# Kernel optimization log

Hardware: AMD Instinct MI355X
Metric: run time of the kernel (lower is better)

Reference implementation:

```python
import jax, jax.numpy as jnp
import numpy as np

E, D, DIM, H, DH, MLP = 8, 6, 512, 8, 64, 512
P, S, NC, B = 4, 32, 10, 128
PD = 3 * P * P          # patch_dim = 48
GRID = S // P           # 8
N = GRID * GRID + 1     # 65 tokens (64 patches + cls)


def setup_inputs() -> dict:
    key = jax.random.key(0)
    ks = iter(jax.random.split(key, 16))
    r = lambda *s: jax.random.normal(next(ks), s, jnp.float32) * 0.02
    z = lambda *s: jnp.zeros(s, jnp.float32)
    o = lambda *s: jnp.ones(s, jnp.float32)
    return dict(
        x=jax.random.normal(next(ks), (B, 3, S, S), jnp.float32),
        gate_w=r(E, 3 * S * S), gate_b=z(E),
        pln1_g=o(E, PD), pln1_b=z(E, PD),
        patch_w=r(E, PD, DIM), patch_b=z(E, DIM),
        pln2_g=o(E, DIM), pln2_b=z(E, DIM),
        cls_tok=r(E, DIM), pos_emb=r(E, N, DIM),
        aln_g=o(E, D, DIM), aln_b=z(E, D, DIM),
        qkv_w=r(E, D, DIM, 3 * H * DH),
        out_w=r(E, D, H * DH, DIM), out_b=z(E, D, DIM),
        fln_g=o(E, D, DIM), fln_b=z(E, D, DIM),
        ff1_w=r(E, D, DIM, MLP), ff1_b=z(E, D, MLP),
        ff2_w=r(E, D, MLP, DIM), ff2_b=z(E, D, DIM),
        final_g=o(E, DIM), final_b=z(E, DIM),
        head_w=r(E, DIM, NC), head_b=z(E, NC))


def _ln(x, g, b):
    m = x.mean(-1, keepdims=True)
    v = ((x - m) ** 2).mean(-1, keepdims=True)
    return (x - m) * jax.lax.rsqrt(v + 1e-5) * g + b


LAYER_KEYS = ('aln_g', 'aln_b', 'qkv_w', 'out_w', 'out_b',
              'fln_g', 'fln_b', 'ff1_w', 'ff1_b', 'ff2_w', 'ff2_b')


def _vit(x, p):
    # x: [B, 3, S, S]; p: per-expert param dict (no leading expert axis)
    Bx = x.shape[0]
    # rearrange 'b c (h p1) (w p2) -> b (h w) (p1 p2 c)'
    t = x.reshape(Bx, 3, GRID, P, GRID, P).transpose(0, 2, 4, 3, 5, 1)
    t = t.reshape(Bx, GRID * GRID, PD)
    t = _ln(t, p['pln1_g'], p['pln1_b'])
    t = t @ p['patch_w'] + p['patch_b']
    t = _ln(t, p['pln2_g'], p['pln2_b'])
    cls = jnp.broadcast_to(p['cls_tok'][None, None, :], (Bx, 1, DIM))
    t = jnp.concatenate([cls, t], axis=1) + p['pos_emb'][None]  # [B, N, DIM]

    def block(t, lp):
        g = _ln(t, lp['aln_g'], lp['aln_b'])
        qkv = g @ lp['qkv_w']                       # [B, N, 3*H*DH]
        q, k, v = jnp.split(qkv, 3, axis=-1)
        q = q.reshape(Bx, N, H, DH).transpose(0, 2, 1, 3)
        k = k.reshape(Bx, N, H, DH).transpose(0, 2, 1, 3)
        v = v.reshape(Bx, N, H, DH).transpose(0, 2, 1, 3)
        att = jax.nn.softmax(jnp.einsum('bhid,bhjd->bhij', q, k) * (DH ** -0.5), axis=-1)
        o = jnp.einsum('bhij,bhjd->bhid', att, v).transpose(0, 2, 1, 3).reshape(Bx, N, H * DH)
        t = t + o @ lp['out_w'] + lp['out_b']
        g = _ln(t, lp['fln_g'], lp['fln_b'])
        f = jax.nn.gelu(g @ lp['ff1_w'] + lp['ff1_b'], approximate=False) @ lp['ff2_w'] + lp['ff2_b']
        return t + f, None

    layer_p = {k: p[k] for k in LAYER_KEYS}  # each [D, ...]
    t, _ = jax.lax.scan(block, t, layer_p)
    t = _ln(t, p['final_g'], p['final_b'])
    return t[:, 0] @ p['head_w'] + p['head_b']   # [B, NC]


def _moe(x, params):
    Bx = x.shape[0]
    logits = x.reshape(Bx, -1) @ params['gate_w'].T + params['gate_b']  # [B, E]
    top1 = jnp.argmax(logits, axis=1)                                   # [B]
    expert_p = {k: v for k, v in params.items() if k not in ('gate_w', 'gate_b')}
    all_out = jax.vmap(lambda pp: _vit(x, pp))(expert_p)                # [E, B, NC]
    return all_out[top1, jnp.arange(Bx)]                                # [B, NC]


def reference(x, gate_w, gate_b, pln1_g, pln1_b, patch_w, patch_b, pln2_g, pln2_b,
              cls_tok, pos_emb, aln_g, aln_b, qkv_w, out_w, out_b,
              fln_g, fln_b, ff1_w, ff1_b, ff2_w, ff2_b, final_g, final_b,
              head_w, head_b):
    params = {k: v for k, v in locals().items() if k != 'x'}
    return _moe(x, params)
```

## Files before the change

### kernel.cpp

```cpp
#include <hip/hip_runtime.h>
#include <math.h>

#define EXPERTS 8
#define DEPTH 6
#define DIM 512
#define HEADS 8
#define NCLS 10
#define BATCH 128
#define PD 48
#define NTOK 65
#define NRT256 40
#define NRT128 80
#define NROWSP (NRT256 * 256)

typedef __attribute__((ext_vector_type(4))) float f32x4;
typedef __attribute__((ext_vector_type(8))) __bf16 bf16x8;
typedef unsigned short u16;

#define GLOAD_LDS16(gp, lp)                                                     \
    __builtin_amdgcn_global_load_lds(                                           \
        (const __attribute__((address_space(1))) void*)(gp),                    \
        (__attribute__((address_space(3))) void*)(lp), 16, 0, 0)

__device__ inline u16 f2bf(float f) {
    union { float f; unsigned u; } v; v.f = f;
    unsigned r = v.u + 0x7FFFu + ((v.u >> 16) & 1u);
    return (u16)(r >> 16);
}
__device__ inline float bf2f(u16 s) {
    union { unsigned u; float f; } v; v.u = ((unsigned)s) << 16;
    return v.f;
}

__global__ __launch_bounds__(256) void gate_k(const float* __restrict__ x,
                                              const float* __restrict__ gw,
                                              const float* __restrict__ gb,
                                              int* __restrict__ top1) {
    int b = blockIdx.x, tid = threadIdx.x;
    const float* xb = x + (size_t)b * 3072;
    float acc[EXPERTS];
#pragma unroll
    for (int e = 0; e < EXPERTS; ++e) acc[e] = 0.f;
    for (int i = tid; i < 3072; i += 256) {
        float xv = xb[i];
#pragma unroll
        for (int e = 0; e < EXPERTS; ++e)
            acc[e] = fmaf(xv, gw[(size_t)e * 3072 + i], acc[e]);
    }
    __shared__ float red[256];
    __shared__ float logits[EXPERTS];
    for (int e = 0; e < EXPERTS; ++e) {
        red[tid] = acc[e];
        __syncthreads();
        for (int s = 128; s > 0; s >>= 1) {
            if (tid < s) red[tid] += red[tid + s];
            __syncthreads();
        }
        if (tid == 0) logits[e] = red[0] + gb[e];
        __syncthreads();
    }
    if (tid == 0) {
        int best = 0;
        float bv = logits[0];
        for (int e = 1; e < EXPERTS; ++e)
            if (logits[e] > bv) { bv = logits[e]; best = e; }
        top1[b] = best;
    }
}

__global__ __launch_bounds__(128) void route3_k(const int* __restrict__ top1,
                                                int* __restrict__ prow,
                                                int* __restrict__ tile_e) {
    __shared__ int t1[BATCH];
    int tid = threadIdx.x;
    t1[tid] = top1[tid];
    __syncthreads();
    if (tid != 0) return;
    int row = 0, tile = 0;
    for (int e = 0; e < EXPERTS; ++e) {
        int ne = 0;
        for (int b = 0; b < BATCH; ++b)
            if (t1[b] == e) { prow[b] = row + ne * 65; ne++; }
        if (!ne) continue;
        int nt = (ne * 65 + 255) >> 8;
        for (int tt = 0; tt < nt; ++tt) tile_e[tile++] = e;
        row += nt << 8;
    }
    for (; tile < NRT256; ++tile) tile_e[tile] = -1;
}

__global__ __launch_bounds__(256) void patch_k(const float* __restrict__ x,
                                               const float* __restrict__ pln1_g,
                                               const float* __restrict__ pln1_b,
                                               const float* __restrict__ patch_w,
                                               const float* __restrict__ patch_b,
                                               const float* __restrict__ pln2_g,
                                               const float* __restrict__ pln2_b,
                                               const float* __restrict__ cls_tok,
                                               const float* __restrict__ pos_emb,
                                               const int* __restrict__ top1,
                                               const int* __restrict__ prow,
                                               float* __restrict__ t) {
    int n = blockIdx.x, b = blockIdx.y, tid = threadIdx.x;
    int e = top1[b];
    float* trow = t + ((size_t)prow[b] + n) * DIM;
    const float* pe = pos_emb + ((size_t)e * NTOK + n) * DIM;

    if (n == 0) {
        for (int d = tid; d < DIM; d += 256)
            trow[d] = cls_tok[e * DIM + d] + pe[d];
        return;
    }
    int pi = n - 1, h = pi >> 3, w = pi & 7;
    __shared__ float pv[PD];
    __shared__ float red[256];
    if (tid < PD) {
        int p1 = tid / 12, rem = tid % 12, p2 = rem / 3, c = rem % 3;
        pv[tid] = x[((size_t)b * 3 + c) * 1024 + (h * 4 + p1) * 32 + (w * 4 + p2)];
    }
    __syncthreads();
    float m = 0.f, q = 0.f;
    for (int j = 0; j < PD; ++j) { float v = pv[j]; m += v; q += v * v; }
    m *= (1.f / PD);
    q = q * (1.f / PD) - m * m;
    float rs = rsqrtf(q + 1e-5f);
    __syncthreads();
    if (tid < PD)
        pv[tid] = (pv[tid] - m) * rs * pln1_g[e * PD + tid] + pln1_b[e * PD + tid];
    __syncthreads();

    float acc0 = patch_b[e * DIM + tid];
    float acc1 = patch_b[e * DIM + tid + 256];
    for (int j = 0; j < PD; ++j) {
        float v = pv[j];
        const float* wr = patch_w + ((size_t)e * PD + j) * DIM;
        acc0 = fmaf(v, wr[tid], acc0);
        acc1 = fmaf(v, wr[tid + 256], acc1);
    }
    red[tid] = acc0 + acc1;
    __syncthreads();
    for (int s = 128; s > 0; s >>= 1) {
        if (tid < s) red[tid] += red[tid + s];
        __syncthreads();
    }
    float S = red[0];
    __syncthreads();
    red[tid] = acc0 * acc0 + acc1 * acc1;
    __syncthreads();
    for (int s = 128; s > 0; s >>= 1) {
        if (tid < s) red[tid] += red[tid + s];
        __syncthreads();
    }
    float Q = red[0];
    float mean = S * (1.f / DIM);
    float var = Q * (1.f / DIM) - mean * mean;
    float rs2 = rsqrtf(var + 1e-5f);
    trow[tid]       = (acc0 - mean) * rs2 * pln2_g[e * DIM + tid]       + pln2_b[e * DIM + tid]       + pe[tid];
    trow[tid + 256] = (acc1 - mean) * rs2 * pln2_g[e * DIM + tid + 256] + pln2_b[e * DIM + tid + 256] + pe[tid + 256];
}

__global__ __launch_bounds__(256) void ln2_k(const float* __restrict__ src,
                                             u16* __restrict__ dst,
                                             const float* __restrict__ gbase,
                                             const float* __restrict__ bbase,
                                             const int* __restrict__ tile_e,
                                             int gestride) {
    int row = blockIdx.x * 4 + (threadIdx.x >> 6);
    int lane = threadIdx.x & 63;
    int e = tile_e[row >> 8];
    if (e < 0) return;
    const float* s = src + (size_t)row * 512;
    float4 a = *(const float4*)&s[lane * 4];
    float4 b = *(const float4*)&s[256 + lane * 4];
    float sum = a.x + a.y + a.z + a.w + b.x + b.y + b.z + b.w;
    float sq = a.x * a.x + a.y * a.y + a.z * a.z + a.w * a.w +
               b.x * b.x + b.y * b.y + b.z * b.z + b.w * b.w;
#pragma unroll
    for (int off = 32; off > 0; off >>= 1) {
        sum += __shfl_xor(sum, off);
        sq += __shfl_xor(sq, off);
    }
    float mean = sum * (1.f / DIM);
    float rs = rsqrtf(sq * (1.f / DIM) - mean * mean + 1e-5f);
    const float* g = gbase + (size_t)e * gestride;
    const float* bb = bbase + (size_t)e * gestride;
    float4 g0 = *(const float4*)&g[lane * 4];
    float4 g1 = *(const float4*)&g[256 + lane * 4];
    float4 b0 = *(const float4*)&bb[lane * 4];
    float4 b1 = *(const float4*)&bb[256 + lane * 4];
    int swz = (row & 7) << 3;
    u16 o[4];
    o[0] = f2bf((a.x - mean) * rs * g0.x + b0.x);
    o[1] = f2bf((a.y - mean) * rs * g0.y + b0.y);
    o[2] = f2bf((a.z - mean) * rs * g0.z + b0.z);
    o[3] = f2bf((a.w - mean) * rs * g0.w + b0.w);
    *(int2*)&dst[(size_t)row * 512 + ((lane * 4) ^ swz)] = *(int2*)o;
    o[0] = f2bf((b.x - mean) * rs * g1.x + b1.x);
    o[1] = f2bf((b.y - mean) * rs * g1.y + b1.y);
    o[2] = f2bf((b.z - mean) * rs * g1.z + b1.z);
    o[3] = f2bf((b.w - mean) * rs * g1.w + b1.w);
    *(int2*)&dst[(size_t)row * 512 + ((256 + lane * 4) ^ swz)] = *(int2*)o;
}

__global__ __launch_bounds__(256) void wconv_k(const float* __restrict__ src,
                                               u16* __restrict__ dst, int N) {
    __shared__ float tile[32][33];
    int n0 = blockIdx.x * 32, k0 = blockIdx.y * 32, m = blockIdx.z;
    const float* s = src + (size_t)m * 512 * N;
    u16* d = dst + (size_t)m * 512 * N;
    int r = threadIdx.x >> 5, c = threadIdx.x & 31;
#pragma unroll
    for (int i = 0; i < 4; ++i)
        tile[r + i * 8][c] = s[(size_t)(k0 + r + i * 8) * N + n0 + c];
    __syncthreads();
#pragma unroll
    for (int i = 0; i < 4; ++i) {
        int n = n0 + r + i * 8;
        d[(size_t)n * 512 + ((k0 + c) ^ ((n & 7) << 3))] = f2bf(tile[c][r + i * 8]);
    }
}

__global__ __launch_bounds__(512) void mgemm6_k(const u16* __restrict__ A,
                                                const u16* __restrict__ Wtbase,
                                                u16* __restrict__ C,
                                                const int* __restrict__ tile_e,
                                                int westride) {
    constexpr int N = 1536, CT = 12;
    int orig = blockIdx.x, nwg = NRT256 * CT;
    int q = nwg >> 3, r8 = nwg & 7;
    int xcd = orig & 7, off = orig >> 3;
    int wg = (xcd < r8 ? xcd * (q + 1) : r8 * (q + 1) + (xcd - r8) * q) + off;
    int tile = wg / CT, ct = wg - tile * CT;
    int e = tile_e[tile];
    if (e < 0) return;
    int row0 = tile * 256, c0 = ct * 128;
    const u16* Wt = Wtbase + (size_t)e * westride;

    int tid = threadIdx.x;
    int lane = tid & 63, w = tid >> 6;
    int rl = lane & 15, kg = lane >> 4;
    int wr = w >> 1, wc = w & 1;

    __shared__ __align__(16) u16 As[256 * 64];
    __shared__ __align__(16) u16 Bs[128 * 64];

    f32x4 acc[4][4];
#pragma unroll
    for (int mt = 0; mt < 4; ++mt)
#pragma unroll
        for (int nt = 0; nt < 4; ++nt) acc[mt][nt] = (f32x4){0.f, 0.f, 0.f, 0.f};

    const u16* Ag = A + (size_t)(row0 + w * 32 + (lane >> 3)) * 512 + (lane & 7) * 8;
    const u16* Bg = Wt + (size_t)(c0 + w * 16 + (lane >> 3)) * 512 + (lane & 7) * 8;
    u16* Asw = As + w * 2048;
    u16* Bsw = Bs + w * 1024;

    int blk0 = (kg ^ (rl & 7)) * 8;
    int blk1 = ((4 + kg) ^ (rl & 7)) * 8;

    for (int k0 = 0; k0 < 512; k0 += 64) {
#pragma unroll
        for (int i = 0; i < 4; ++i)
            GLOAD_LDS16(Ag + k0 + i * 8 * 512, Asw + i * 512);
#pragma unroll
        for (int i = 0; i < 2; ++i)
            GLOAD_LDS16(Bg + k0 + i * 8 * 512, Bsw + i * 512);
        __syncthreads();
#pragma unroll
        for (int ks = 0; ks < 2; ++ks) {
            int blk = ks ? blk1 : blk0;
            bf16x8 av[4], bv[4];
#pragma unroll
            for (int i = 0; i < 4; ++i) {
                av[i] = *(const bf16x8*)&As[(wr * 64 + i * 16 + rl) * 64 + blk];
                bv[i] = *(const bf16x8*)&Bs[(wc * 64 + i * 16 + rl) * 64 + blk];
            }
#pragma unroll
            for (int mt = 0; mt < 4; ++mt)
#pragma unroll
                for (int nt = 0; nt < 4; ++nt)
                    acc[mt][nt] = __builtin_amdgcn_mfma_f32_16x16x32_bf16(
                        av[mt], bv[nt], acc[mt][nt], 0, 0, 0);
        }
        __syncthreads();
    }

    int rh = lane >> 4;
#pragma unroll
    for (int mt = 0; mt < 4; ++mt)
#pragma unroll
        for (int nt = 0; nt < 4; ++nt)
#pragma unroll
            for (int rr = 0; rr < 4; ++rr) {
                size_t grow = row0 + wr * 64 + mt * 16 + rh * 4 + rr;
                int c = c0 + wc * 64 + nt * 16 + rl;
                C[grow * N + c] = f2bf(acc[mt][nt][rr]);
            }
}

template <int OP>
__global__ __launch_bounds__(256) void mgemm5_k(const u16* __restrict__ A,
                                                const u16* __restrict__ Wtbase,
                                                const float* __restrict__ Bbase,
                                                void* __restrict__ Cptr,
                                                const int* __restrict__ tile_e,
                                                int westride, int bestride) {
    constexpr int CT = 4;
    int orig = blockIdx.x, nwg = NRT128 * CT;
    int q = nwg >> 3, r8 = nwg & 7;
    int xcd = orig & 7, off = orig >> 3;
    int wg = (xcd < r8 ? xcd * (q + 1) : r8 * (q + 1) + (xcd - r8) * q) + off;
    int tile = wg / CT, ct = wg - tile * CT;
    int e = tile_e[tile >> 1];
    if (e < 0) return;
    int row0 = tile * 128, c0 = ct * 128;
    const u16* Wt = Wtbase + (size_t)e * westride;

    int tid = threadIdx.x;
    int lane = tid & 63, w = tid >> 6;
    int rl = lane & 15, kg = lane >> 4;
    int wr = w >> 1, wc = w & 1;

    __shared__ __align__(16) u16 As[128 * 64];
    __shared__ __align__(16) u16 Bs[128 * 64];

    f32x4 acc[4][4];
#pragma unroll
    for (int mt = 0; mt < 4; ++mt)
#pragma unroll
        for (int nt = 0; nt < 4; ++nt) acc[mt][nt] = (f32x4){0.f, 0.f, 0.f, 0.f};

    const u16* Ag = A + (size_t)(row0 + w * 32 + (lane >> 3)) * 512 + (lane & 7) * 8;
    const u16* Bg = Wt + (size_t)(c0 + w * 32 + (lane >> 3)) * 512 + (lane & 7) * 8;
    u16* Asw = As + w * 2048;
    u16* Bsw = Bs + w * 2048;

    int blk0 = (kg ^ (rl & 7)) * 8;
    int blk1 = ((4 + kg) ^ (rl & 7)) * 8;

    for (int k0 = 0; k0 < 512; k0 += 64) {
#pragma unroll
        for (int i = 0; i < 4; ++i) {
            GLOAD_LDS16(Ag + k0 + i * 8 * 512, Asw + i * 512);
            GLOAD_LDS16(Bg + k0 + i * 8 * 512, Bsw + i * 512);
        }
        __syncthreads();
#pragma unroll
        for (int ks = 0; ks < 2; ++ks) {
            int blk = ks ? blk1 : blk0;
            bf16x8 av[4], bv[4];
#pragma unroll
            for (int i = 0; i < 4; ++i) {
                av[i] = *(const bf16x8*)&As[(wr * 64 + i * 16 + rl) * 64 + blk];
                bv[i] = *(const bf16x8*)&Bs[(wc * 64 + i * 16 + rl) * 64 + blk];
            }
#pragma unroll
            for (int mt = 0; mt < 4; ++mt)
#pragma unroll
                for (int nt = 0; nt < 4; ++nt)
                    acc[mt][nt] = __builtin_amdgcn_mfma_f32_16x16x32_bf16(
                        av[mt], bv[nt], acc[mt][nt], 0, 0, 0);
        }
        __syncthreads();
    }

    int rh = lane >> 4;
#pragma unroll
    for (int mt = 0; mt < 4; ++mt)
#pragma unroll
        for (int nt = 0; nt < 4; ++nt)
#pragma unroll
            for (int rr = 0; rr < 4; ++rr) {
                size_t grow = row0 + wr * 64 + mt * 16 + rh * 4 + rr;
                int c = c0 + wc * 64 + nt * 16 + rl;
                float v = acc[mt][nt][rr];
                if (OP == 1) {
                    ((float*)Cptr)[grow * 512 + c] += v + Bbase[(size_t)e * bestride + c];
                } else {
                    float vb = v + Bbase[(size_t)e * bestride + c];
                    float gl = vb * 0.5f * (1.f + erff(vb * 0.70710678118f));
                    ((u16*)Cptr)[grow * 512 + (c ^ (((int)grow & 7) << 3))] = f2bf(gl);
                }
            }
}

#define ATT_LDS (23040 / 2 + 8320 / 2 + 12288 / 2)
__global__ __launch_bounds__(320) void attn3_k(const u16* __restrict__ qkv,
                                               u16* __restrict__ o,
                                               const int* __restrict__ prow) {
    int h = blockIdx.x, b = blockIdx.y, tid = threadIdx.x;
    int pr = prow[b];
    __shared__ __align__(16) u16 smem[ATT_LDS];
    u16* Qs = smem;
    u16* Ks = smem + 80 * 72;
    u16* Ps = smem;
    u16* Vs = smem + 2 * 80 * 72;
    u16* Vt = Vs + 65 * 64;

    const u16* base = qkv + (size_t)pr * 1536 + h * 64;

    for (int idx = tid; idx < 640; idx += 320) {
        int r = idx >> 3, q = idx & 7;
        int4 vq = {0, 0, 0, 0}, vk = {0, 0, 0, 0};
        if (r < NTOK) {
            vq = *(const int4*)&base[(size_t)r * 1536 + q * 8];
            vk = *(const int4*)&base[(size_t)r * 1536 + 512 + q * 8];
        }
        *(int4*)&Qs[r * 72 + q * 8] = vq;
        *(int4*)&Ks[r * 72 + q * 8] = vk;
    }
    for (int idx = tid; idx < 520; idx += 320) {
        int r = idx >> 3, q = idx & 7;
        *(int4*)&Vs[r * 64 + q * 8] = *(const int4*)&base[(size_t)r * 1536 + 1024 + q * 8];
    }
    __syncthreads();

    int lane = tid & 63, mt = tid >> 6;
    int rl = lane & 15, kg = lane >> 4, g = lane >> 4;

    f32x4 acc[5];
#pragma unroll
    for (int nt = 0; nt < 5; ++nt) acc[nt] = (f32x4){0.f, 0.f, 0.f, 0.f};

    {
        bf16x8 av0 = *(const bf16x8*)&Qs[(mt * 16 + rl) * 72 + kg * 8];
        bf16x8 av1 = *(const bf16x8*)&Qs[(mt * 16 + rl) * 72 + 32 + kg * 8];
#pragma unroll
        for (int nt = 0; nt < 5; ++nt) {
            bf16x8 bv0 = *(const bf16x8*)&Ks[(nt * 16 + rl) * 72 + kg * 8];
            bf16x8 bv1 = *(const bf16x8*)&Ks[(nt * 16 + rl) * 72 + 32 + kg * 8];
            acc[nt] = __builtin_amdgcn_mfma_f32_16x16x32_bf16(av0, bv0, acc[nt], 0, 0, 0);
            acc[nt] = __builtin_amdgcn_mfma_f32_16x16x32_bf16(av1, bv1, acc[nt], 0, 0, 0);
        }
    }

    for (int idx = tid; idx < 768; idx += 320) {
        int d = idx & 63, kq = idx >> 6;
        u16 tmp[8];
#pragma unroll
        for (int j = 0; j < 8; ++j) {
            int k = kq * 8 + j;
            tmp[j] = (k < NTOK) ? Vs[k * 64 + d] : (u16)0;
        }
        *(int4*)&Vt[d * 96 + kq * 8] = *(int4*)tmp;
    }

#pragma unroll
    for (int r = 0; r < 4; ++r) {
        float m = -3.0e38f;
#pragma unroll
        for (int nt = 0; nt < 5; ++nt) {
            float s = acc[nt][r] * 0.125f;
            if (nt * 16 + rl >= NTOK) s = -3.0e38f;
            acc[nt][r] = s;
            m = fmaxf(m, s);
        }
        m = fmaxf(m, __shfl_xor(m, 1));
        m = fmaxf(m, __shfl_xor(m, 2));
        m = fmaxf(m, __shfl_xor(m, 4));
        m = fmaxf(m, __shfl_xor(m, 8));
        float sum = 0.f;
#pragma unroll
        for (int nt = 0; nt < 5; ++nt) {
            float p = expf(acc[nt][r] - m);
            acc[nt][r] = p;
            sum += p;
        }
        sum += __shfl_xor(sum, 1);
        sum += __shfl_xor(sum, 2);
        sum += __shfl_xor(sum, 4);
        sum += __shfl_xor(sum, 8);
        float inv = 1.f / sum;
#pragma unroll
        for (int nt = 0; nt < 5; ++nt) acc[nt][r] *= inv;
    }
    __syncthreads();

#pragma unroll
    for (int nt = 0; nt < 5; ++nt)
#pragma unroll
        for (int r = 0; r < 4; ++r)
            Ps[(mt * 16 + g * 4 + r) * 96 + nt * 16 + rl] = f2bf(acc[nt][r]);
    for (int idx = tid; idx < 160; idx += 320) {
        int r = idx >> 1, hf = idx & 1;
        *(int4*)&Ps[r * 96 + 80 + hf * 8] = (int4){0, 0, 0, 0};
    }
    __syncthreads();

#pragma unroll
    for (int dt = 0; dt < 4; ++dt) {
        f32x4 oa = {0.f, 0.f, 0.f, 0.f};
#pragma unroll
        for (int s2 = 0; s2 < 3; ++s2) {
            bf16x8 av = *(const bf16x8*)&Ps[(mt * 16 + rl) * 96 + s2 * 32 + kg * 8];
            bf16x8 bv = *(const bf16x8*)&Vt[(dt * 16 + rl) * 96 + s2 * 32 + kg * 8];
            oa = __builtin_amdgcn_mfma_f32_16x16x32_bf16(av, bv, oa, 0, 0, 0);
        }
#pragma unroll
        for (int r = 0; r < 4; ++r) {
            int row = mt * 16 + g * 4 + r;
            if (row < NTOK) {
                int grow = pr + row;
                int c = h * 64 + dt * 16 + rl;
                o[(size_t)grow * DIM + (c ^ ((grow & 7) << 3))] = f2bf(oa[r]);
            }
        }
    }
}

__global__ __launch_bounds__(64) void final_k(const float* __restrict__ t,
                                              const float* __restrict__ fg,
                                              const float* __restrict__ fb,
                                              const float* __restrict__ hw,
                                              const float* __restrict__ hb,
                                              const int* __restrict__ top1,
                                              const int* __restrict__ prow,
                                              float* __restrict__ out) {
    int b = blockIdx.x, lane = threadIdx.x;
    int e = top1[b];
    const float* row = t + (size_t)prow[b] * DIM;
    float v[8], s = 0.f, q = 0.f;
#pragma unroll
    for (int ii = 0; ii < 8; ++ii) {
        v[ii] = row[ii * 64 + lane];
        s += v[ii];
        q += v[ii] * v[ii];
    }
    for (int off = 32; off > 0; off >>= 1) {
        s += __shfl_xor(s, off);
        q += __shfl_xor(q, off);
    }
    float mean = s * (1.f / DIM);
    float var = q * (1.f / DIM) - mean * mean;
    float rs = rsqrtf(var + 1e-5f);
    float nv[8];
#pragma unroll
    for (int ii = 0; ii < 8; ++ii) {
        int d = ii * 64 + lane;
        nv[ii] = (v[ii] - mean) * rs * fg[e * DIM + d] + fb[e * DIM + d];
    }
    for (int c = 0; c < NCLS; ++c) {
        float p = 0.f;
#pragma unroll
        for (int ii = 0; ii < 8; ++ii) {
            int d = ii * 64 + lane;
            p = fmaf(nv[ii], hw[(size_t)e * DIM * NCLS + d * NCLS + c], p);
        }
        for (int off = 32; off > 0; off >>= 1) p += __shfl_xor(p, off);
        if (lane == 0) out[b * NCLS + c] = p + hb[e * NCLS + c];
    }
}

extern "C" void kernel_launch(void* const* d_in, const int* in_sizes, int n_in,
                              void* d_out, int out_size, void* d_ws, size_t ws_size,
                              hipStream_t stream) {
    const float* x       = (const float*)d_in[0];
    const float* gate_w  = (const float*)d_in[1];
    const float* gate_b  = (const float*)d_in[2];
    const float* pln1_g  = (const float*)d_in[3];
    const float* pln1_b  = (const float*)d_in[4];
    const float* patch_w = (const float*)d_in[5];
    const float* patch_b = (const float*)d_in[6];
    const float* pln2_g  = (const float*)d_in[7];
    const float* pln2_b  = (const float*)d_in[8];
    const float* cls_tok = (const float*)d_in[9];
    const float* pos_emb = (const float*)d_in[10];
    const float* aln_g   = (const float*)d_in[11];
    const float* aln_b   = (const float*)d_in[12];
    const float* qkv_w   = (const float*)d_in[13];
    const float* out_w   = (const float*)d_in[14];
    const float* out_b   = (const float*)d_in[15];
    const float* fln_g   = (const float*)d_in[16];
    const float* fln_b   = (const float*)d_in[17];
    const float* ff1_w   = (const float*)d_in[18];
    const float* ff1_b   = (const float*)d_in[19];
    const float* ff2_w   = (const float*)d_in[20];
    const float* ff2_b   = (const float*)d_in[21];
    const float* final_g = (const float*)d_in[22];
    const float* final_b = (const float*)d_in[23];
    const float* head_w  = (const float*)d_in[24];
    const float* head_b  = (const float*)d_in[25];
    float* out = (float*)d_out;

    int* top1   = (int*)d_ws;
    int* prow   = top1 + 128;
    int* tile_e = prow + 128;
    float* t  = (float*)((char*)d_ws + 4096);
    u16* aln  = (u16*)(t + (size_t)NROWSP * DIM);
    u16* qb16 = aln + (size_t)NROWSP * DIM;
    u16* ao16 = qb16 + (size_t)NROWSP * 1536;
    u16* h16  = ao16 + (size_t)NROWSP * DIM;
    u16* wq_t = h16 + (size_t)NROWSP * DIM;
    u16* wo_t = wq_t + (size_t)48 * 1536 * 512;
    u16* w1_t = wo_t + (size_t)48 * 512 * 512;
    u16* w2_t = w1_t + (size_t)48 * 512 * 512;

    gate_k<<<BATCH, 256, 0, stream>>>(x, gate_w, gate_b, top1);
    route3_k<<<1, 128, 0, stream>>>(top1, prow, tile_e);
    patch_k<<<dim3(NTOK, BATCH), 256, 0, stream>>>(x, pln1_g, pln1_b, patch_w, patch_b,
                                                   pln2_g, pln2_b, cls_tok, pos_emb,
                                                   top1, prow, t);
    wconv_k<<<dim3(48, 16, 48), 256, 0, stream>>>(qkv_w, wq_t, 1536);
    wconv_k<<<dim3(16, 16, 48), 256, 0, stream>>>(out_w, wo_t, 512);
    wconv_k<<<dim3(16, 16, 48), 256, 0, stream>>>(ff1_w, w1_t, 512);
    wconv_k<<<dim3(16, 16, 48), 256, 0, stream>>>(ff2_w, w2_t, 512);

    for (int l = 0; l < DEPTH; ++l) {
        ln2_k<<<NROWSP / 4, 256, 0, stream>>>(t, aln, aln_g + l * DIM, aln_b + l * DIM,
                                              tile_e, DEPTH * DIM);
        mgemm6_k<<<NRT256 * 12, 512, 0, stream>>>(
            aln, wq_t + (size_t)l * 1536 * 512, qb16, tile_e, DEPTH * 512 * 1536);
        attn3_k<<<dim3(HEADS, BATCH), 320, 0, stream>>>(qb16, ao16, prow);
        mgemm5_k<1><<<NRT128 * 4, 256, 0, stream>>>(
            ao16, wo_t + (size_t)l * 512 * 512, out_b + l * DIM, t, tile_e,
            DEPTH * 512 * 512, DEPTH * DIM);
        ln2_k<<<NROWSP / 4, 256, 0, stream>>>(t, aln, fln_g + l * DIM, fln_b + l * DIM,
                                              tile_e, DEPTH * DIM);
        mgemm5_k<2><<<NRT128 * 4, 256, 0, stream>>>(
            aln, w1_t + (size_t)l * 512 * 512, ff1_b + l * DIM, h16, tile_e,
            DEPTH * 512 * 512, DEPTH * DIM);
        mgemm5_k<1><<<NRT128 * 4, 256, 0, stream>>>(
            h16, w2_t + (size_t)l * 512 * 512, ff2_b + l * DIM, t, tile_e,
            DEPTH * 512 * 512, DEPTH * DIM);
    }
    final_k<<<BATCH, 64, 0, stream>>>(t, final_g, final_b, head_w, head_b, top1, prow, out);
}
```

Before: 863.3 us.

## Fuse residual-add GEMMs with following LayerNorm and merge weight conversions

Adds a full-row GEMM kernel (32 rows x 512 cols per block) that adds bias and residual into T, then computes the row LayerNorm in the epilogue using cross-wave reductions and writes the normalized bf16 activation for the next GEMM. This removes the two standalone LN kernels per layer and their extra reads of T. It also merges three weight-conversion launches into one. In exchange, the new GEMM uses narrow 32-row tiles with a large 64KB B tile in LDS and no double buffering, which can lower occupancy and weight reuse.

```diff
diff --git a/kernel.cpp b/kernel.cpp
--- a/kernel.cpp
+++ b/kernel.cpp
@@ -11,6 +11,7 @@
 #define NTOK 65
 #define NRT256 40
 #define NRT128 80
+#define NRT32 (NRT256 * 8)
 #define NROWSP (NRT256 * 256)
 
 typedef __attribute__((ext_vector_type(4))) float f32x4;
@@ -202,13 +203,11 @@
     *(int2*)&dst[(size_t)row * 512 + ((256 + lane * 4) ^ swz)] = *(int2*)o;
 }
 
-__global__ __launch_bounds__(256) void wconv_k(const float* __restrict__ src,
-                                               u16* __restrict__ dst, int N) {
+__device__ inline void wconv_body(const float* __restrict__ s,
+                                  u16* __restrict__ d, int N,
+                                  int n0, int k0, int tid) {
     __shared__ float tile[32][33];
-    int n0 = blockIdx.x * 32, k0 = blockIdx.y * 32, m = blockIdx.z;
-    const float* s = src + (size_t)m * 512 * N;
-    u16* d = dst + (size_t)m * 512 * N;
-    int r = threadIdx.x >> 5, c = threadIdx.x & 31;
+    int r = tid >> 5, c = tid & 31;
 #pragma unroll
     for (int i = 0; i < 4; ++i)
         tile[r + i * 8][c] = s[(size_t)(k0 + r + i * 8) * N + n0 + c];
@@ -218,6 +217,25 @@
         int n = n0 + r + i * 8;
         d[(size_t)n * 512 + ((k0 + c) ^ ((n & 7) << 3))] = f2bf(tile[c][r + i * 8]);
     }
+}
+
+__global__ __launch_bounds__(256) void wconv_k(const float* __restrict__ src,
+                                               u16* __restrict__ dst, int N) {
+    wconv_body(src + (size_t)blockIdx.z * 512 * N, dst + (size_t)blockIdx.z * 512 * N,
+               N, blockIdx.x * 32, blockIdx.y * 32, threadIdx.x);
+}
+
+__global__ __launch_bounds__(256) void wconv3_k(const float* __restrict__ s0,
+                                                const float* __restrict__ s1,
+                                                const float* __restrict__ s2,
+                                                u16* __restrict__ d0,
+                                                u16* __restrict__ d1,
+                                                u16* __restrict__ d2) {
+    int z = blockIdx.z, which = z / 48, m = z % 48;
+    const float* s = (which == 0) ? s0 : (which == 1) ? s1 : s2;
+    u16* d = (which == 0) ? d0 : (which == 1) ? d1 : d2;
+    wconv_body(s + (size_t)m * 512 * 512, d + (size_t)m * 512 * 512,
+               512, blockIdx.x * 32, blockIdx.y * 32, threadIdx.x);
 }
 
 __global__ __launch_bounds__(512) void mgemm6_k(const u16* __restrict__ A,
@@ -298,13 +316,12 @@
             }
 }
 
-template <int OP>
-__global__ __launch_bounds__(256) void mgemm5_k(const u16* __restrict__ A,
-                                                const u16* __restrict__ Wtbase,
-                                                const float* __restrict__ Bbase,
-                                                void* __restrict__ Cptr,
-                                                const int* __restrict__ tile_e,
-                                                int westride, int bestride) {
+__global__ __launch_bounds__(256) void mgemm5g_k(const u16* __restrict__ A,
+                                                 const u16* __restrict__ Wtbase,
+                                                 const float* __restrict__ Bbase,
+                                                 u16* __restrict__ C,
+                                                 const int* __restrict__ tile_e,
+                                                 int westride, int bestride) {
     constexpr int CT = 4;
     int orig = blockIdx.x, nwg = NRT128 * CT;
     int q = nwg >> 3, r8 = nwg & 7;
@@ -373,15 +390,129 @@
             for (int rr = 0; rr < 4; ++rr) {
                 size_t grow = row0 + wr * 64 + mt * 16 + rh * 4 + rr;
                 int c = c0 + wc * 64 + nt * 16 + rl;
-                float v = acc[mt][nt][rr];
-                if (OP == 1) {
-                    ((float*)Cptr)[grow * 512 + c] += v + Bbase[(size_t)e * bestride + c];
-                } else {
-                    float vb = v + Bbase[(size_t)e * bestride + c];
-                    float gl = vb * 0.5f * (1.f + erff(vb * 0.70710678118f));
-                    ((u16*)Cptr)[grow * 512 + (c ^ (((int)grow & 7) << 3))] = f2bf(gl);
+                float vb = acc[mt][nt][rr] + Bbase[(size_t)e * bestride + c];
+                float gl = vb * 0.5f * (1.f + erff(vb * 0.70710678118f));
+                C[grow * 512 + (c ^ (((int)grow & 7) << 3))] = f2bf(gl);
+            }
+}
+
+template <int LNMODE>
+__global__ __launch_bounds__(256) void gemmres_k(const u16* __restrict__ A,
+                                                 const u16* __restrict__ Wtbase,
+                                                 const float* __restrict__ Bbase,
+                                                 float* __restrict__ T,
+                                                 const float* __restrict__ gbase,
+                                                 const float* __restrict__ bbase2,
+                                                 u16* __restrict__ dst,
+                                                 const int* __restrict__ tile_e,
+                                                 int westride, int bestride,
+                                                 int gestride) {
+    int orig = blockIdx.x;
+    int wg = (orig & 7) * (NRT32 >> 3) + (orig >> 3);
+    int e = tile_e[wg >> 3];
+    if (e < 0) return;
+    int row0 = wg * 32;
+    const u16* Wt = Wtbase + (size_t)e * westride;
+
+    int tid = threadIdx.x;
+    int lane = tid & 63, w = tid >> 6;
+    int rl = lane & 15, kg = lane >> 4, rh = lane >> 4;
+
+    __shared__ __align__(16) u16 As[32 * 64];
+    __shared__ __align__(16) u16 Bs[512 * 64];
+    __shared__ float redS[4][32], redQ[4][32];
+
+    f32x4 acc[2][8];
+#pragma unroll
+    for (int mt = 0; mt < 2; ++mt)
+#pragma unroll
+        for (int nt = 0; nt < 8; ++nt) acc[mt][nt] = (f32x4){0.f, 0.f, 0.f, 0.f};
+
+    const u16* Ag = A + (size_t)(row0 + w * 8 + (lane >> 3)) * 512 + (lane & 7) * 8;
+    const u16* Bg = Wt + (size_t)(w * 128 + (lane >> 3)) * 512 + (lane & 7) * 8;
+    u16* Asw = As + w * 512;
+    u16* Bsw = Bs + w * 8192;
+
+    int blk0 = (kg ^ (rl & 7)) * 8;
+    int blk1 = ((4 + kg) ^ (rl & 7)) * 8;
+
+    for (int k0 = 0; k0 < 512; k0 += 64) {
+        GLOAD_LDS16(Ag + k0, Asw);
+#pragma unroll
+        for (int i = 0; i < 16; ++i)
+            GLOAD_LDS16(Bg + k0 + i * 8 * 512, Bsw + i * 512);
+        __syncthreads();
+#pragma unroll
+        for (int ks = 0; ks < 2; ++ks) {
+            int blk = ks ? blk1 : blk0;
+            bf16x8 av[2], bv[8];
+#pragma unroll
+            for (int i = 0; i < 2; ++i)
+                av[i] = *(const bf16x8*)&As[(i * 16 + rl) * 64 + blk];
+#pragma unroll
+            for (int i = 0; i < 8; ++i)
+                bv[i] = *(const bf16x8*)&Bs[(w * 128 + i * 16 + rl) * 64 + blk];
+#pragma unroll
+            for (int mt = 0; mt < 2; ++mt)
+#pragma unroll
+                for (int nt = 0; nt < 8; ++nt)
+                    acc[mt][nt] = __builtin_amdgcn_mfma_f32_16x16x32_bf16(
+                        av[mt], bv[nt], acc[mt][nt], 0, 0, 0);
+        }
+        __syncthreads();
+    }
+
+    float bias_nt[8];
+#pragma unroll
+    for (int nt = 0; nt < 8; ++nt)
+        bias_nt[nt] = Bbase[(size_t)e * bestride + w * 128 + nt * 16 + rl];
+
+#pragma unroll
+    for (int mt = 0; mt < 2; ++mt)
+#pragma unroll
+        for (int rr = 0; rr < 4; ++rr) {
+            int rowl = mt * 16 + rh * 4 + rr;
+            size_t grow = row0 + rowl;
+            float s = 0.f, q = 0.f;
+#pragma unroll
+            for (int nt = 0; nt < 8; ++nt) {
+                int c = w * 128 + nt * 16 + rl;
+                float tv = T[grow * 512 + c] + acc[mt][nt][rr] + bias_nt[nt];
+                acc[mt][nt][rr] = tv;
+                s += tv;
+                q += tv * tv;
+            }
+            s += __shfl_xor(s, 1); q += __shfl_xor(q, 1);
+            s += __shfl_xor(s, 2); q += __shfl_xor(q, 2);
+            s += __shfl_xor(s, 4); q += __shfl_xor(q, 4);
+            s += __shfl_xor(s, 8); q += __shfl_xor(q, 8);
+            if (rl == 0) { redS[w][rowl] = s; redQ[w][rowl] = q; }
+        }
+    __syncthreads();
+
+#pragma unroll
+    for (int mt = 0; mt < 2; ++mt)
+#pragma unroll
+        for (int rr = 0; rr < 4; ++rr) {
+            int rowl = mt * 16 + rh * 4 + rr;
+            size_t grow = row0 + rowl;
+            float S = redS[0][rowl] + redS[1][rowl] + redS[2][rowl] + redS[3][rowl];
+            float Q = redQ[0][rowl] + redQ[1][rowl] + redQ[2][rowl] + redQ[3][rowl];
+            float mean = S * (1.f / DIM);
+            float rs = rsqrtf(Q * (1.f / DIM) - mean * mean + 1e-5f);
+            int swz = ((int)grow & 7) << 3;
+#pragma unroll
+            for (int nt = 0; nt < 8; ++nt) {
+                int c = w * 128 + nt * 16 + rl;
+                float tv = acc[mt][nt][rr];
+                T[grow * 512 + c] = tv;
+                if (LNMODE) {
+                    float g = gbase[(size_t)e * gestride + c];
+                    float b2 = bbase2[(size_t)e * gestride + c];
+                    dst[grow * 512 + (c ^ swz)] = f2bf((tv - mean) * rs * g + b2);
                 }
             }
+        }
 }
 
 #define ATT_LDS (23040 / 2 + 8320 / 2 + 12288 / 2)
@@ -587,7 +718,8 @@
     int* tile_e = prow + 128;
     float* t  = (float*)((char*)d_ws + 4096);
     u16* aln  = (u16*)(t + (size_t)NROWSP * DIM);
-    u16* qb16 = aln + (size_t)NROWSP * DIM;
+    u16* fln  = aln + (size_t)NROWSP * DIM;
+    u16* qb16 = fln + (size_t)NROWSP * DIM;
     u16* ao16 = qb16 + (size_t)NROWSP * 1536;
     u16* h16  = ao16 + (size_t)NROWSP * DIM;
     u16* wq_t = h16 + (size_t)NROWSP * DIM;
@@ -601,27 +733,31 @@
                                                    pln2_g, pln2_b, cls_tok, pos_emb,
                                                    top1, prow, t);
     wconv_k<<<dim3(48, 16, 48), 256, 0, stream>>>(qkv_w, wq_t, 1536);
-    wconv_k<<<dim3(16, 16, 48), 256, 0, stream>>>(out_w, wo_t, 512);
-    wconv_k<<<dim3(16, 16, 48), 256, 0, stream>>>(ff1_w, w1_t, 512);
-    wconv_k<<<dim3(16, 16, 48), 256, 0, stream>>>(ff2_w, w2_t, 512);
+    wconv3_k<<<dim3(16, 16, 144), 256, 0, stream>>>(out_w, ff1_w, ff2_w, wo_t, w1_t, w2_t);
+
+    ln2_k<<<NROWSP / 4, 256, 0, stream>>>(t, aln, aln_g, aln_b, tile_e, DEPTH * DIM);
 
     for (int l = 0; l < DEPTH; ++l) {
-        ln2_k<<<NROWSP / 4, 256, 0, stream>>>(t, aln, aln_g + l * DIM, aln_b + l * DIM,
-                                              tile_e, DEPTH * DIM);
         mgemm6_k<<<NRT256 * 12, 512, 0, stream>>>(
             aln, wq_t + (size_t)l * 1536 * 512, qb16, tile_e, DEPTH * 512 * 1536);
         attn3_k<<<dim3(HEADS, BATCH), 320, 0, stream>>>(qb16, ao16, prow);
-        mgemm5_k<1><<<NRT128 * 4, 256, 0, stream>>>(
-            ao16, wo_t + (size_t)l * 512 * 512, out_b + l * DIM, t, tile_e,
+        gemmres_k<1><<<NRT32, 256, 0, stream>>>(
+            ao16, wo_t + (size_t)l * 512 * 512, out_b + l * DIM, t,
+            fln_g + l * DIM, fln_b + l * DIM, fln, tile_e,
+            DEPTH * 512 * 512, DEPTH * DIM, DEPTH * DIM);
+        mgemm5g_k<<<NRT128 * 4, 256, 0, stream>>>(
+            fln, w1_t + (size_t)l * 512 * 512, ff1_b + l * DIM, h16, tile_e,
             DEPTH * 512 * 512, DEPTH * DIM);
-        ln2_k<<<NROWSP / 4, 256, 0, stream>>>(t, aln, fln_g + l * DIM, fln_b + l * DIM,
-                                              tile_e, DEPTH * DIM);
-        mgemm5_k<2><<<NRT128 * 4, 256, 0, stream>>>(
-            aln, w1_t + (size_t)l * 512 * 512, ff1_b + l * DIM, h16, tile_e,
-            DEPTH * 512 * 512, DEPTH * DIM);
-        mgemm5_k<1><<<NRT128 * 4, 256, 0, stream>>>(
-            h16, w2_t + (size_t)l * 512 * 512, ff2_b + l * DIM, t, tile_e,
-            DEPTH * 512 * 512, DEPTH * DIM);
+        if (l < DEPTH - 1)
+            gemmres_k<1><<<NRT32, 256, 0, stream>>>(
+                h16, w2_t + (size_t)l * 512 * 512, ff2_b + l * DIM, t,
+                aln_g + (l + 1) * DIM, aln_b + (l + 1) * DIM, aln, tile_e,
+                DEPTH * 512 * 512, DEPTH * DIM, DEPTH * DIM);
+        else
+            gemmres_k<0><<<NRT32, 256, 0, stream>>>(
+                h16, w2_t + (size_t)l * 512 * 512, ff2_b + l * DIM, t,
+                aln_g, aln_b, aln, tile_e,
+                DEPTH * 512 * 512, DEPTH * DIM, DEPTH * DIM);
     }
     final_k<<<BATCH, 64, 0, stream>>>(t, final_g, final_b, head_w, head_b, top1, prow, out);
 }
```

Result: slower. 1.100 ms (+27.4%).

## Fuse weight fp32-to-bf16 transpose into GEMM B-tile staging, drop wconv pass

Applied to the files above, without the earlier changes.

Removes the separate wconv_k kernels that transposed and converted every expert's weights to swizzled bf16 before the layer loop. The GEMM kernels now read fp32 weights directly with float4 loads, convert them to bf16 and write them transposed into the swizzled LDS tile. This avoids a full-weight conversion pass (about 48 weight matrices per kind) and its extra global traffic. In exchange, each GEMM reads twice the bytes for weights, repeats the conversion per row tile, and uses register-staged stores instead of direct global-to-LDS loads. The attention grid is also flattened so that consecutive blocks cover different batch items.

```diff
diff --git a/kernel.cpp b/kernel.cpp
--- a/kernel.cpp
+++ b/kernel.cpp
@@ -26,10 +26,6 @@
     union { float f; unsigned u; } v; v.f = f;
     unsigned r = v.u + 0x7FFFu + ((v.u >> 16) & 1u);
     return (u16)(r >> 16);
-}
-__device__ inline float bf2f(u16 s) {
-    union { unsigned u; float f; } v; v.u = ((unsigned)s) << 16;
-    return v.f;
 }
 
 __global__ __launch_bounds__(256) void gate_k(const float* __restrict__ x,
@@ -202,26 +198,29 @@
     *(int2*)&dst[(size_t)row * 512 + ((256 + lane * 4) ^ swz)] = *(int2*)o;
 }
 
-__global__ __launch_bounds__(256) void wconv_k(const float* __restrict__ src,
-                                               u16* __restrict__ dst, int N) {
-    __shared__ float tile[32][33];
-    int n0 = blockIdx.x * 32, k0 = blockIdx.y * 32, m = blockIdx.z;
-    const float* s = src + (size_t)m * 512 * N;
-    u16* d = dst + (size_t)m * 512 * N;
-    int r = threadIdx.x >> 5, c = threadIdx.x & 31;
-#pragma unroll
-    for (int i = 0; i < 4; ++i)
-        tile[r + i * 8][c] = s[(size_t)(k0 + r + i * 8) * N + n0 + c];
-    __syncthreads();
+template <int NSTRIDE>
+__device__ inline void stage_b_fp32(const float* __restrict__ W, int k0, int c0,
+                                    u16* __restrict__ Bs, int nb, int kq) {
+    float4 wv[4];
+#pragma unroll
+    for (int j = 0; j < 4; ++j)
+        wv[j] = *(const float4*)&W[(size_t)(k0 + kq * 4 + j) * NSTRIDE + c0 + nb * 4];
+    int kk = kq * 4;
+    int kbase = (kk & ~7), klo = kk & 7;
 #pragma unroll
     for (int i = 0; i < 4; ++i) {
-        int n = n0 + r + i * 8;
-        d[(size_t)n * 512 + ((k0 + c) ^ ((n & 7) << 3))] = f2bf(tile[c][r + i * 8]);
+        int n = nb * 4 + i;
+        u16 t4[4];
+        t4[0] = f2bf(((const float*)&wv[0])[i]);
+        t4[1] = f2bf(((const float*)&wv[1])[i]);
+        t4[2] = f2bf(((const float*)&wv[2])[i]);
+        t4[3] = f2bf(((const float*)&wv[3])[i]);
+        *(int2*)&Bs[n * 64 + (kbase ^ ((n & 7) << 3)) + klo] = *(int2*)t4;
     }
 }
 
 __global__ __launch_bounds__(512) void mgemm6_k(const u16* __restrict__ A,
-                                                const u16* __restrict__ Wtbase,
+                                                const float* __restrict__ Wbase,
                                                 u16* __restrict__ C,
                                                 const int* __restrict__ tile_e,
                                                 int westride) {
@@ -234,7 +233,7 @@
     int e = tile_e[tile];
     if (e < 0) return;
     int row0 = tile * 256, c0 = ct * 128;
-    const u16* Wt = Wtbase + (size_t)e * westride;
+    const float* W = Wbase + (size_t)e * westride;
 
     int tid = threadIdx.x;
     int lane = tid & 63, w = tid >> 6;
@@ -251,9 +250,8 @@
         for (int nt = 0; nt < 4; ++nt) acc[mt][nt] = (f32x4){0.f, 0.f, 0.f, 0.f};
 
     const u16* Ag = A + (size_t)(row0 + w * 32 + (lane >> 3)) * 512 + (lane & 7) * 8;
-    const u16* Bg = Wt + (size_t)(c0 + w * 16 + (lane >> 3)) * 512 + (lane & 7) * 8;
     u16* Asw = As + w * 2048;
-    u16* Bsw = Bs + w * 1024;
+    int nb = tid & 31, kq = tid >> 5;
 
     int blk0 = (kg ^ (rl & 7)) * 8;
     int blk1 = ((4 + kg) ^ (rl & 7)) * 8;
@@ -262,9 +260,7 @@
 #pragma unroll
         for (int i = 0; i < 4; ++i)
             GLOAD_LDS16(Ag + k0 + i * 8 * 512, Asw + i * 512);
-#pragma unroll
-        for (int i = 0; i < 2; ++i)
-            GLOAD_LDS16(Bg + k0 + i * 8 * 512, Bsw + i * 512);
+        stage_b_fp32<1536>(W, k0, c0, Bs, nb, kq);
         __syncthreads();
 #pragma unroll
         for (int ks = 0; ks < 2; ++ks) {
@@ -300,7 +296,7 @@
 
 template <int OP>
 __global__ __launch_bounds__(256) void mgemm5_k(const u16* __restrict__ A,
-                                                const u16* __restrict__ Wtbase,
+                                                const float* __restrict__ Wbase,
                                                 const float* __restrict__ Bbase,
                                                 void* __restrict__ Cptr,
                                                 const int* __restrict__ tile_e,
@@ -314,7 +310,7 @@
     int e = tile_e[tile >> 1];
     if (e < 0) return;
     int row0 = tile * 128, c0 = ct * 128;
-    const u16* Wt = Wtbase + (size_t)e * westride;
+    const float* W = Wbase + (size_t)e * westride;
 
     int tid = threadIdx.x;
     int lane = tid & 63, w = tid >> 6;
@@ -331,19 +327,19 @@
         for (int nt = 0; nt < 4; ++nt) acc[mt][nt] = (f32x4){0.f, 0.f, 0.f, 0.f};
 
     const u16* Ag = A + (size_t)(row0 + w * 32 + (lane >> 3)) * 512 + (lane & 7) * 8;
-    const u16* Bg = Wt + (size_t)(c0 + w * 32 + (lane >> 3)) * 512 + (lane & 7) * 8;
     u16* Asw = As + w * 2048;
-    u16* Bsw = Bs + w * 2048;
+    int nb = tid & 31, kb = tid >> 5;
 
     int blk0 = (kg ^ (rl & 7)) * 8;
     int blk1 = ((4 + kg) ^ (rl & 7)) * 8;
 
     for (int k0 = 0; k0 < 512; k0 += 64) {
 #pragma unroll
-        for (int i = 0; i < 4; ++i) {
+        for (int i = 0; i < 4; ++i)
             GLOAD_LDS16(Ag + k0 + i * 8 * 512, Asw + i * 512);
-            GLOAD_LDS16(Bg + k0 + i * 8 * 512, Bsw + i * 512);
-        }
+#pragma unroll
+        for (int h = 0; h < 2; ++h)
+            stage_b_fp32<512>(W, k0, c0, Bs, nb, h * 8 + kb);
         __syncthreads();
 #pragma unroll
         for (int ks = 0; ks < 2; ++ks) {
@@ -388,7 +384,7 @@
 __global__ __launch_bounds__(320) void attn3_k(const u16* __restrict__ qkv,
                                                u16* __restrict__ o,
                                                const int* __restrict__ prow) {
-    int h = blockIdx.x, b = blockIdx.y, tid = threadIdx.x;
+    int b = blockIdx.x & 127, h = blockIdx.x >> 7, tid = threadIdx.x;
     int pr = prow[b];
     __shared__ __align__(16) u16 smem[ATT_LDS];
     u16* Qs = smem;
@@ -590,37 +586,30 @@
     u16* qb16 = aln + (size_t)NROWSP * DIM;
     u16* ao16 = qb16 + (size_t)NROWSP * 1536;
     u16* h16  = ao16 + (size_t)NROWSP * DIM;
-    u16* wq_t = h16 + (size_t)NROWSP * DIM;
-    u16* wo_t = wq_t + (size_t)48 * 1536 * 512;
-    u16* w1_t = wo_t + (size_t)48 * 512 * 512;
-    u16* w2_t = w1_t + (size_t)48 * 512 * 512;
 
     gate_k<<<BATCH, 256, 0, stream>>>(x, gate_w, gate_b, top1);
     route3_k<<<1, 128, 0, stream>>>(top1, prow, tile_e);
     patch_k<<<dim3(NTOK, BATCH), 256, 0, stream>>>(x, pln1_g, pln1_b, patch_w, patch_b,
                                                    pln2_g, pln2_b, cls_tok, pos_emb,
                                                    top1, prow, t);
-    wconv_k<<<dim3(48, 16, 48), 256, 0, stream>>>(qkv_w, wq_t, 1536);
-    wconv_k<<<dim3(16, 16, 48), 256, 0, stream>>>(out_w, wo_t, 512);
-    wconv_k<<<dim3(16, 16, 48), 256, 0, stream>>>(ff1_w, w1_t, 512);
-    wconv_k<<<dim3(16, 16, 48), 256, 0, stream>>>(ff2_w, w2_t, 512);
 
     for (int l = 0; l < DEPTH; ++l) {
         ln2_k<<<NROWSP / 4, 256, 0, stream>>>(t, aln, aln_g + l * DIM, aln_b + l * DIM,
                                               tile_e, DEPTH * DIM);
         mgemm6_k<<<NRT256 * 12, 512, 0, stream>>>(
-            aln, wq_t + (size_t)l * 1536 * 512, qb16, tile_e, DEPTH * 512 * 1536);
-        attn3_k<<<dim3(HEADS, BATCH), 320, 0, stream>>>(qb16, ao16, prow);
+            aln, qkv_w + (size_t)l * 512 * 1536, qb16, tile_e,
+            DEPTH * 512 * 1536);
+        attn3_k<<<HEADS * BATCH, 320, 0, stream>>>(qb16, ao16, prow);
         mgemm5_k<1><<<NRT128 * 4, 256, 0, stream>>>(
-            ao16, wo_t + (size_t)l * 512 * 512, out_b + l * DIM, t, tile_e,
+            ao16, out_w + (size_t)l * 512 * 512, out_b + l * DIM, t, tile_e,
             DEPTH * 512 * 512, DEPTH * DIM);
         ln2_k<<<NROWSP / 4, 256, 0, stream>>>(t, aln, fln_g + l * DIM, fln_b + l * DIM,
                                               tile_e, DEPTH * DIM);
         mgemm5_k<2><<<NRT128 * 4, 256, 0, stream>>>(
-            aln, w1_t + (size_t)l * 512 * 512, ff1_b + l * DIM, h16, tile_e,
+            aln, ff1_w + (size_t)l * 512 * 512, ff1_b + l * DIM, h16, tile_e,
             DEPTH * 512 * 512, DEPTH * DIM);
         mgemm5_k<1><<<NRT128 * 4, 256, 0, stream>>>(
-            h16, w2_t + (size_t)l * 512 * 512, ff2_b + l * DIM, t, tile_e,
+            h16, ff2_w + (size_t)l * 512 * 512, ff2_b + l * DIM, t, tile_e,
             DEPTH * 512 * 512, DEPTH * DIM);
     }
     final_k<<<BATCH, 64, 0, stream>>>(t, final_g, final_b, head_w, head_b, top1, prow, out);
```

Result: slower. 972.5 us (+12.6%).
